# Performance work log

Measured on AMD Instinct MI355X. Metric: run time of the kernel, lower is better.

The kernel has to match this reference:

```python
import jax, jax.numpy as jnp
import numpy as np

C = 64  # num_channels
B, H, W = 16, 160, 160


def squeeze2d(x, f=2):
    b, c, h, w = x.shape
    x = x.reshape(b, c, h // f, f, w // f, f)
    x = x.transpose(0, 1, 3, 5, 2, 4)
    return x.reshape(b, c * f * f, h // f, w // f)


def unsqueeze2d(x, f=2):
    b, c, h, w = x.shape
    x = x.reshape(b, c // (f * f), f, f, h, w)
    x = x.transpose(0, 1, 4, 2, 5, 3)
    return x.reshape(b, c // (f * f), h * f, w * f)


def get_indices(num_channels):
    # generate_ind(p) tiles the row-major-flattened 2x2 pattern over C//4 channel groups
    def gen(p):
        return np.tile(np.array(p, dtype=bool), num_channels // 4)
    m = np.ones(num_channels, dtype=bool)
    t = gen([0, 0, 1, 1]); b = ~t
    l = gen([0, 1, 0, 1]); r = ~l
    return (m, t, b, l, r, t & l, t & r, b & l, b & r)


INDS = get_indices(C)


def conv1x1(z, w):
    # 1x1 conv == channel matmul
    return jnp.einsum('oc,bchw->bohw', w, z)


def partition_input(x):
    z = unsqueeze2d(x)
    z = jnp.pad(z, ((0, 0), (0, 0), (1, 1), (1, 1)), constant_values=-1.0)
    z = squeeze2d(z)  # (B, C, H+1, W+1)
    m, t, b, l, r, tl, tr, bl, br = INDS
    return (z[:, :, 1:-1, 1:-1],
            z[:, t, :1, 1:-1], z[:, b, -1:, 1:-1],
            z[:, l, 1:-1, :1], z[:, r, 1:-1, -1:],
            z[:, tl, :1, :1], z[:, tr, :1, -1:],
            z[:, bl, -1:, :1], z[:, br, -1:, -1:])


def unsqueeze_line(ze):
    b, c = ze.shape[:2]
    sz = (1, -1) if ze.shape[-2] == 1 else (-1, 1)
    return ze.reshape(b, c // 2, 2, -1).transpose(0, 1, 3, 2).reshape(b, c // 2, *sz)


def merge_output(z_m, z_t, z_b, z_l, z_r, z_tl, z_tr, z_bl, z_br):
    z_m = unsqueeze2d(z_m)
    z_t, z_b, z_l, z_r = [unsqueeze_line(zi) for zi in (z_t, z_b, z_l, z_r)]
    z_tt = jnp.concatenate([z_tl, z_t, z_tr], axis=3)
    z_mm = jnp.concatenate([z_l, z_m, z_r], axis=3)
    z_bb = jnp.concatenate([z_bl, z_b, z_br], axis=3)
    return squeeze2d(jnp.concatenate([z_tt, z_mm, z_bb], axis=2))


def setup_inputs() -> dict:
    key = jax.random.key(0)
    k1, k2 = jax.random.split(key)
    x = jax.random.normal(k1, (B, C, H, W), dtype=jnp.float32)
    logdet = jax.random.normal(k2, (B,), dtype=jnp.float32)
    rng = np.random.RandomState(0)
    w_init = np.linalg.qr(rng.randn(C, C))[0].astype(np.float32)
    weight = jnp.asarray(w_init)
    return {"input": x, "logdet": logdet, "weight": weight}


def reference(input, logdet, weight):
    h, w = input.shape[-2:]
    pixels = [(h - 1) * (w - 1), w - 1, w - 1, h - 1, h - 1, 1, 1, 1, 1]
    ws = [weight[np.ix_(ind, ind)] for ind in INDS]
    dlogdet = sum(jnp.linalg.slogdet(wi)[1] * p for wi, p in zip(ws, pixels))
    zs = partition_input(input)
    outs = [conv1x1(z, wi) for z, wi in zip(zs, ws)]
    output = merge_output(*outs)
    return output, logdet + dlogdet
```

## Files before the change

### kernel.cpp

```cpp
#include <hip/hip_runtime.h>
#include <math.h>

#define NB 16
#define NC 64
#define HW 160
#define PLANE (HW * HW)
#define SG 161
#define SGSQ (SG * SG)
#define NSITES (NB * SGSQ)
#define OUT_LD_OFF (NB * NC * PLANE)
#define TILE 256
#define NCONV ((NSITES + TILE - 1) / TILE)

#define SMEM_FLOATS (32 * 256)

__device__ inline int chmap(int i, int n, int pa, int pb) {
    if (n == 64) return i;
    if (n == 32) return ((i >> 1) << 2) | ((i & 1) ? pb : pa);
    return (i << 2) | pa;
}

__device__ float wave_lu_logabsdet(const float* __restrict__ W, float* A,
                                   int n, int sh, int pa, int pb, int lane) {
    for (int e = lane; e < n * n; e += 64) {
        int i = e >> sh, j = e & (n - 1);
        A[e] = W[chmap(i, n, pa, pb) * 64 + chmap(j, n, pa, pb)];
    }
    asm volatile("s_waitcnt lgkmcnt(0) vmcnt(0)" ::: "memory");
    float logdet = 0.f;
    for (int k = 0; k < n; ++k) {
        float cand = -1.f;
        int idx = k;
        if (lane >= k && lane < n) {
            cand = fabsf(A[(lane << sh) + k]);
            idx = lane;
        }
        for (int off = 32; off; off >>= 1) {
            float oc = __shfl_down(cand, off, 64);
            int oi = __shfl_down(idx, off, 64);
            if (oc > cand) { cand = oc; idx = oi; }
        }
        int p = __shfl(idx, 0, 64);
        if (p != k && lane < n) {
            float tk = A[(k << sh) + lane];
            float tp = A[(p << sh) + lane];
            A[(k << sh) + lane] = tp;
            A[(p << sh) + lane] = tk;
        }
        asm volatile("s_waitcnt lgkmcnt(0)" ::: "memory");
        float piv = A[(k << sh) + k];
        logdet += logf(fabsf(piv));
        float rpiv = 1.f / piv;
        float ckj = (lane < n) ? A[(k << sh) + lane] : 0.f;
        bool act = (lane > k) && (lane < n);
        for (int i2 = k + 1; i2 < n; ++i2) {
            float aik = A[(i2 << sh) + k];
            float mult = aik * rpiv;
            if (act) A[(i2 << sh) + lane] = fmaf(-mult, ckj, A[(i2 << sh) + lane]);
        }
        asm volatile("s_waitcnt lgkmcnt(0)" ::: "memory");
    }
    return logdet;
}

__global__ __launch_bounds__(256, 4) void InvConv1x1GridAlign_kernel(
    const float* __restrict__ x, const float* __restrict__ ld_in,
    const float* __restrict__ W, float* __restrict__ out) {
    __shared__ __align__(16) float smem[SMEM_FLOATS];
    const int tid = threadIdx.x;

    if (blockIdx.x == 0) {
        float* A64 = smem;
        float* A32a = smem + 4096;
        float* A32b = smem + 5120;
        float* A16 = smem + 6144;
        float* partial = smem + 6400;
        int wid = tid >> 6;
        int lane = tid & 63;
        float part = 0.f;
        if (wid == 0) {
            part = 25281.f * wave_lu_logabsdet(W, A64, 64, 6, 0, 0, lane);
        } else if (wid == 1) {
            part  = wave_lu_logabsdet(W, A32a, 32, 5, 2, 3, lane);
            part += wave_lu_logabsdet(W, A32a, 32, 5, 0, 1, lane);
            part *= 159.f;
        } else if (wid == 2) {
            part  = wave_lu_logabsdet(W, A32b, 32, 5, 1, 3, lane);
            part += wave_lu_logabsdet(W, A32b, 32, 5, 0, 2, lane);
            part *= 159.f;
        } else {
            part  = wave_lu_logabsdet(W, A16, 16, 4, 3, 0, lane);
            part += wave_lu_logabsdet(W, A16, 16, 4, 2, 0, lane);
            part += wave_lu_logabsdet(W, A16, 16, 4, 1, 0, lane);
            part += wave_lu_logabsdet(W, A16, 16, 4, 0, 0, lane);
        }
        if (lane == 0) partial[wid] = part;
        __syncthreads();
        if (tid < NB) {
            float dl = partial[0] + partial[1] + partial[2] + partial[3];
            out[OUT_LD_OFF + tid] = ld_in[tid] + dl;
        }
        return;
    }

    const int tile0 = ((int)blockIdx.x - 1) * TILE;
    const int lane = tid & 63;
    const int wid = tid >> 6;
    const int wo = __builtin_amdgcn_readfirstlane(wid << 4);

    const int offm[4] = {0, 1, HW, HW + 1};
    bool vm[4];
    int baseoff;
    const float* xb;
    {
        int s = tile0 + tid;
        bool sok = s < NSITES;
        unsigned us = (unsigned)(sok ? s : 0);
        unsigned b = us / SGSQ;
        unsigned rr = us - b * SGSQ;
        unsigned Y = rr / SG;
        unsigned X = rr - Y * SG;
        xb = x + (size_t)b * (NC * PLANE);
        baseoff = ((int)Y - 1) * HW + ((int)X - 1);
        bool okT = sok && (Y >= 1), okB = sok && (Y <= HW - 1);
        bool okL = (X >= 1), okR = (X <= HW - 1);
        vm[0] = okT && okL; vm[1] = okT && okR;
        vm[2] = okB && okL; vm[3] = okB && okR;
    }

    float acc[16][4];
#pragma unroll
    for (int j = 0; j < 16; ++j)
#pragma unroll
        for (int s2 = 0; s2 < 4; ++s2) acc[j][s2] = 0.f;

#pragma unroll 1
    for (int half = 0; half < 2; ++half) {
        __syncthreads();
#pragma unroll 8
        for (int krow = 0; krow < 32; ++krow) {
            const int k = (half << 5) + krow;
            const int pl = k ^ 3;
            const int m = krow & 3;
            float val = vm[m] ? xb[pl * PLANE + baseoff + offm[m]] : 0.f;
            smem[(krow << 8) + tid] = val;
        }
        __syncthreads();
#pragma unroll 1
        for (int kb = 0; kb < 8; ++kb) {
            float v[4][4];
            const float* vb = smem + (kb << 10) + lane;
#pragma unroll
            for (int kk = 0; kk < 4; ++kk)
#pragma unroll
                for (int s2 = 0; s2 < 4; ++s2)
                    v[kk][s2] = vb[(kk << 8) + (s2 << 6)];
            const int k0 = (half << 5) + (kb << 2);
#pragma unroll
            for (int jb = 0; jb < 2; ++jb) {
                float4 w4[8];
#pragma unroll
                for (int j = 0; j < 8; ++j)
                    w4[j] = *(const float4*)(W + (wo + (jb << 3) + j) * 64 + k0);
#pragma unroll
                for (int j = 0; j < 8; ++j) {
                    const int jj = (jb << 3) + j;
#pragma unroll
                    for (int kk = 0; kk < 4; ++kk) {
                        const float wjk = (kk == 0) ? w4[j].x
                                        : (kk == 1) ? w4[j].y
                                        : (kk == 2) ? w4[j].z : w4[j].w;
#pragma unroll
                        for (int s2 = 0; s2 < 4; ++s2)
                            acc[jj][s2] = fmaf(wjk, v[kk][s2], acc[jj][s2]);
                    }
                }
            }
        }
    }

#pragma unroll
    for (int s2 = 0; s2 < 4; ++s2) {
        int s = tile0 + lane + (s2 << 6);
        bool sok = s < NSITES;
        unsigned us = (unsigned)(sok ? s : 0);
        unsigned b = us / SGSQ;
        unsigned rr = us - b * SGSQ;
        unsigned Y = rr / SG;
        unsigned X = rr - Y * SG;
        float* ob = out + (size_t)b * (NC * PLANE);
        int boff = ((int)Y - 1) * HW + ((int)X - 1);
        bool okT = sok && (Y >= 1), okB = sok && (Y <= HW - 1);
        bool okL = (X >= 1), okR = (X <= HW - 1);
        bool wm[4] = {okT && okL, okT && okR, okB && okL, okB && okR};
#pragma unroll
        for (int j = 0; j < 16; ++j) {
            const int o = wo + j;
            const int pl = o ^ 3;
            const int m = j & 3;
            if (wm[m]) ob[pl * PLANE + boff + offm[m]] = acc[j][s2];
        }
    }
}

extern "C" void kernel_launch(void* const* d_in, const int* in_sizes, int n_in,
                              void* d_out, int out_size, void* d_ws, size_t ws_size,
                              hipStream_t stream) {
    const float* x = (const float*)d_in[0];
    const float* ld = (const float*)d_in[1];
    const float* W = (const float*)d_in[2];
    float* out = (float*)d_out;
    hipLaunchKernelGGL(InvConv1x1GridAlign_kernel, dim3(NCONV + 1), dim3(256), 0,
                       stream, x, ld, W, out);
}
```

Baseline: 262.5 us.

## Prefetch next input chunk into registers while computing current chunk

Splits the 64-channel reduction into four 16-channel chunks instead of two 32-channel halves. The next chunk's global loads go into registers before the current chunk's FMA loop, so load latency overlaps compute. Loads become branchless by clamping masked addresses to 0 and multiplying by a 0/1 mask, and shared memory shrinks to about 25 KB, which may allow more blocks per CU. The cost is 16 extra live registers and twice as many barrier pairs.

Result: slower. 268.0 us (+2.1%).

```diff
diff --git a/kernel.cpp b/kernel.cpp
--- a/kernel.cpp
+++ b/kernel.cpp
@@ -12,7 +12,7 @@
 #define TILE 256
 #define NCONV ((NSITES + TILE - 1) / TILE)
 
-#define SMEM_FLOATS (32 * 256)
+#define SMEM_FLOATS 6404
 
 __device__ inline int chmap(int i, int n, int pa, int pb) {
     if (n == 64) return i;
@@ -108,11 +108,11 @@
     const int wid = tid >> 6;
     const int wo = __builtin_amdgcn_readfirstlane(wid << 4);
 
-    const int offm[4] = {0, 1, HW, HW + 1};
-    bool vm[4];
-    int baseoff;
+    int aoffm[4];
+    float msk[4];
     const float* xb;
     {
+        const int offm[4] = {0, 1, HW, HW + 1};
         int s = tile0 + tid;
         bool sok = s < NSITES;
         unsigned us = (unsigned)(sok ? s : 0);
@@ -121,11 +121,15 @@
         unsigned Y = rr / SG;
         unsigned X = rr - Y * SG;
         xb = x + (size_t)b * (NC * PLANE);
-        baseoff = ((int)Y - 1) * HW + ((int)X - 1);
+        int baseoff = ((int)Y - 1) * HW + ((int)X - 1);
         bool okT = sok && (Y >= 1), okB = sok && (Y <= HW - 1);
         bool okL = (X >= 1), okR = (X <= HW - 1);
-        vm[0] = okT && okL; vm[1] = okT && okR;
-        vm[2] = okB && okL; vm[3] = okB && okR;
+        bool vm[4] = {okT && okL, okT && okR, okB && okL, okB && okR};
+#pragma unroll
+        for (int m = 0; m < 4; ++m) {
+            aoffm[m] = vm[m] ? (baseoff + offm[m]) : 0;
+            msk[m] = vm[m] ? 1.f : 0.f;
+        }
     }
 
     float acc[16][4];
@@ -134,20 +138,30 @@
 #pragma unroll
         for (int s2 = 0; s2 < 4; ++s2) acc[j][s2] = 0.f;
 
+    float rv[16];
+#pragma unroll
+    for (int j = 0; j < 16; ++j) {
+        const int pl = j ^ 3;
+        rv[j] = xb[pl * PLANE + aoffm[j & 3]];
+    }
+
 #pragma unroll 1
-    for (int half = 0; half < 2; ++half) {
+    for (int q = 0; q < 4; ++q) {
         __syncthreads();
-#pragma unroll 8
-        for (int krow = 0; krow < 32; ++krow) {
-            const int k = (half << 5) + krow;
-            const int pl = k ^ 3;
-            const int m = krow & 3;
-            float val = vm[m] ? xb[pl * PLANE + baseoff + offm[m]] : 0.f;
-            smem[(krow << 8) + tid] = val;
-        }
+#pragma unroll
+        for (int j = 0; j < 16; ++j)
+            smem[(j << 8) + tid] = msk[j & 3] * rv[j];
         __syncthreads();
+        if (q < 3) {
+#pragma unroll
+            for (int j = 0; j < 16; ++j) {
+                const int k = ((q + 1) << 4) + j;
+                const int pl = k ^ 3;
+                rv[j] = xb[pl * PLANE + aoffm[j & 3]];
+            }
+        }
 #pragma unroll 1
-        for (int kb = 0; kb < 8; ++kb) {
+        for (int kb = 0; kb < 4; ++kb) {
             float v[4][4];
             const float* vb = smem + (kb << 10) + lane;
 #pragma unroll
@@ -155,7 +169,7 @@
 #pragma unroll
                 for (int s2 = 0; s2 < 4; ++s2)
                     v[kk][s2] = vb[(kk << 8) + (s2 << 6)];
-            const int k0 = (half << 5) + (kb << 2);
+            const int k0 = (q << 4) + (kb << 2);
 #pragma unroll
             for (int jb = 0; jb < 2; ++jb) {
                 float4 w4[8];
@@ -193,6 +207,7 @@
         bool okT = sok && (Y >= 1), okB = sok && (Y <= HW - 1);
         bool okL = (X >= 1), okR = (X <= HW - 1);
         bool wm[4] = {okT && okL, okT && okR, okB && okL, okB && okR};
+        const int offm[4] = {0, 1, HW, HW + 1};
 #pragma unroll
         for (int j = 0; j < 16; ++j) {
             const int o = wo + j;
```

## Compute sub-matrix log-determinants in registers with packed multi-matrix waves

Applied to the files above, without the earlier changes.

Replaces the LDS-based partial-pivot LU in block 0 with a register-resident LU. Each lane holds one matrix row and the pivot search and elimination use cross-lane shuffles. The two 32x32 and the four 16x16 sub-matrices are packed into one wavefront each so they factor at the same time instead of one after another. This is meant to shorten the serial critical path of the log-determinant block, which could otherwise outlast the convolution blocks. It costs more registers (64 floats per lane in the 64x64 case) and many more shuffles per elimination step.

Measured after the change: 435.7 us. 66.0% more time.

```diff
diff --git a/kernel.cpp b/kernel.cpp
--- a/kernel.cpp
+++ b/kernel.cpp
@@ -20,45 +20,37 @@
     return (i << 2) | pa;
 }
 
-__device__ float wave_lu_logabsdet(const float* __restrict__ W, float* A,
-                                   int n, int sh, int pa, int pb, int lane) {
-    for (int e = lane; e < n * n; e += 64) {
-        int i = e >> sh, j = e & (n - 1);
-        A[e] = W[chmap(i, n, pa, pb) * 64 + chmap(j, n, pa, pb)];
-    }
-    asm volatile("s_waitcnt lgkmcnt(0) vmcnt(0)" ::: "memory");
+template <int N>
+__device__ float reg_lu_logabsdet(const float* __restrict__ W, int pa, int pb,
+                                  int lane) {
+    const int r = lane & (N - 1);
+    const int gb = lane & ~(N - 1);
+    const int row = chmap(r, N, pa, pb);
+    float a[N];
+#pragma unroll
+    for (int j = 0; j < N; ++j) a[j] = W[row * 64 + chmap(j, N, pa, pb)];
+
     float logdet = 0.f;
-    for (int k = 0; k < n; ++k) {
-        float cand = -1.f;
-        int idx = k;
-        if (lane >= k && lane < n) {
-            cand = fabsf(A[(lane << sh) + k]);
-            idx = lane;
-        }
-        for (int off = 32; off; off >>= 1) {
-            float oc = __shfl_down(cand, off, 64);
-            int oi = __shfl_down(idx, off, 64);
-            if (oc > cand) { cand = oc; idx = oi; }
-        }
-        int p = __shfl(idx, 0, 64);
-        if (p != k && lane < n) {
-            float tk = A[(k << sh) + lane];
-            float tp = A[(p << sh) + lane];
-            A[(k << sh) + lane] = tp;
-            A[(p << sh) + lane] = tk;
-        }
-        asm volatile("s_waitcnt lgkmcnt(0)" ::: "memory");
-        float piv = A[(k << sh) + k];
-        logdet += logf(fabsf(piv));
-        float rpiv = 1.f / piv;
-        float ckj = (lane < n) ? A[(k << sh) + lane] : 0.f;
-        bool act = (lane > k) && (lane < n);
-        for (int i2 = k + 1; i2 < n; ++i2) {
-            float aik = A[(i2 << sh) + k];
-            float mult = aik * rpiv;
-            if (act) A[(i2 << sh) + lane] = fmaf(-mult, ckj, A[(i2 << sh) + lane]);
-        }
-        asm volatile("s_waitcnt lgkmcnt(0)" ::: "memory");
+    float used = 0.f;
+#pragma unroll
+    for (int k = 0; k < N; ++k) {
+        float cand = (used != 0.f) ? -1.f : fabsf(a[k]);
+        int idx = r;
+#pragma unroll
+        for (int off = N >> 1; off; off >>= 1) {
+            float oc = __shfl_xor(cand, off, N);
+            int oi = __shfl_xor(idx, off, N);
+            if (oc > cand || (oc == cand && oi < idx)) { cand = oc; idx = oi; }
+        }
+        const int src = gb + idx;
+        float apk = __shfl(a[k], src, 64);
+        logdet += logf(fabsf(apk));
+        float rpiv = 1.f / apk;
+        float mult = (used != 0.f || r == idx) ? 0.f : a[k] * rpiv;
+#pragma unroll
+        for (int j = k + 1; j < N; ++j)
+            a[j] = fmaf(-mult, __shfl(a[j], src, 64), a[j]);
+        if (r == idx) used = 1.f;
     }
     return logdet;
 }
@@ -70,29 +62,25 @@
     const int tid = threadIdx.x;
 
     if (blockIdx.x == 0) {
-        float* A64 = smem;
-        float* A32a = smem + 4096;
-        float* A32b = smem + 5120;
-        float* A16 = smem + 6144;
-        float* partial = smem + 6400;
+        float* partial = smem;
         int wid = tid >> 6;
         int lane = tid & 63;
         float part = 0.f;
         if (wid == 0) {
-            part = 25281.f * wave_lu_logabsdet(W, A64, 64, 6, 0, 0, lane);
+            part = 25281.f * reg_lu_logabsdet<64>(W, 0, 0, lane);
         } else if (wid == 1) {
-            part  = wave_lu_logabsdet(W, A32a, 32, 5, 2, 3, lane);
-            part += wave_lu_logabsdet(W, A32a, 32, 5, 0, 1, lane);
-            part *= 159.f;
+            int g = lane >> 5;
+            float ld = reg_lu_logabsdet<32>(W, g ? 0 : 2, g ? 1 : 3, lane);
+            part = (__shfl(ld, 0, 64) + __shfl(ld, 32, 64)) * 159.f;
         } else if (wid == 2) {
-            part  = wave_lu_logabsdet(W, A32b, 32, 5, 1, 3, lane);
-            part += wave_lu_logabsdet(W, A32b, 32, 5, 0, 2, lane);
-            part *= 159.f;
+            int g = lane >> 5;
+            float ld = reg_lu_logabsdet<32>(W, g ? 0 : 1, g ? 2 : 3, lane);
+            part = (__shfl(ld, 0, 64) + __shfl(ld, 32, 64)) * 159.f;
         } else {
-            part  = wave_lu_logabsdet(W, A16, 16, 4, 3, 0, lane);
-            part += wave_lu_logabsdet(W, A16, 16, 4, 2, 0, lane);
-            part += wave_lu_logabsdet(W, A16, 16, 4, 1, 0, lane);
-            part += wave_lu_logabsdet(W, A16, 16, 4, 0, 0, lane);
+            int pa = 3 - (lane >> 4);
+            float ld = reg_lu_logabsdet<16>(W, pa, 0, lane);
+            part = __shfl(ld, 0, 64) + __shfl(ld, 16, 64) +
+                   __shfl(ld, 32, 64) + __shfl(ld, 48, 64);
         }
         if (lane == 0) partial[wid] = part;
         __syncthreads();
```
